# Kernel tuning notes

Hardware: AMD Instinct MI355X
Metric: run time of the kernel (lower is better)

The kernel has to match this reference:

```python
import jax, jax.numpy as jnp
import numpy as np

NUM_USERS = 100000
NUM_ITEMS = 50000
EMB_DIM = 128
NUM_LAYERS = 3
NUM_EDGES = 2000000
BATCH = 8192
REG = 1e-4


def setup_inputs() -> dict:
    key = jax.random.key(0)
    ks = jax.random.split(key, 8)
    N = NUM_USERS + NUM_ITEMS
    user_emb = jax.random.normal(ks[0], (NUM_USERS, EMB_DIM), dtype=jnp.float32) * 0.01
    item_emb = jax.random.normal(ks[1], (NUM_ITEMS, EMB_DIM), dtype=jnp.float32) * 0.01
    edge_row = jax.random.randint(ks[2], (NUM_EDGES,), 0, N, dtype=jnp.int32)
    edge_col = jax.random.randint(ks[3], (NUM_EDGES,), 0, N, dtype=jnp.int32)
    # symmetric-normalized adjacency values are small positives
    edge_val = jax.random.uniform(ks[4], (NUM_EDGES,), dtype=jnp.float32) * 0.1
    user = jax.random.randint(ks[5], (BATCH,), 0, NUM_USERS, dtype=jnp.int32)
    pos = jax.random.randint(ks[6], (BATCH,), 0, NUM_ITEMS, dtype=jnp.int32)
    neg = jax.random.randint(ks[7], (BATCH,), 0, NUM_ITEMS, dtype=jnp.int32)
    return {"user_emb": user_emb, "item_emb": item_emb,
            "edge_row": edge_row, "edge_col": edge_col, "edge_val": edge_val,
            "user": user, "pos": pos, "neg": neg}


def _lightgcn_embedding(user_emb, item_emb, edge_row, edge_col, edge_val):
    N = user_emb.shape[0] + item_emb.shape[0]
    emb = jnp.concatenate([user_emb, item_emb], axis=0)  # [N, D]
    acc = emb
    for _ in range(NUM_LAYERS):
        # SpMM: out[r] += val * emb[c] for each edge (r, c)
        msg = emb[edge_col] * edge_val[:, None]  # [E, D]
        emb = jax.ops.segment_sum(msg, edge_row, num_segments=N)
        acc = acc + emb
    light = acc / jnp.float32(NUM_LAYERS + 1)  # mean over layer outputs
    return light[:NUM_USERS], light[NUM_USERS:]


def reference(user_emb, item_emb, edge_row, edge_col, edge_val, user, pos, neg):
    u_all, i_all = _lightgcn_embedding(user_emb, item_emb, edge_row, edge_col, edge_val)
    u_lat = u_all[user]          # [B, D]
    pos_lat = i_all[pos]
    neg_lat = i_all[neg]
    pos_score = jnp.sum(u_lat * pos_lat, axis=1)
    neg_score = jnp.sum(u_lat * neg_lat, axis=1)
    # L1 regularization on ego (layer-0) embeddings, scalar broadcast onto batch loss
    reg_loss = REG * (jnp.sum(jnp.abs(user_emb[user]))
                      + jnp.sum(jnp.abs(item_emb[pos]))
                      + jnp.sum(jnp.abs(item_emb[neg])))
    batch_loss = jax.nn.softplus(neg_score - pos_score) + reg_loss
    return batch_loss
```

## Files before the change

kernel.cpp:

```cpp
#include <hip/hip_runtime.h>
#include <hip/hip_bf16.h>

#define EMB_D 128
#define BSH 9
#define MAXBUCK 512
#define CHUNKP 4096

typedef float f32x2 __attribute__((ext_vector_type(2)));

__device__ __forceinline__ float bf16_raw_to_f(unsigned short h) {
    return __uint_as_float(((unsigned int)h) << 16);
}
__device__ __forceinline__ float sane(float v) {
    return (v == v && fabsf(v) < 256.0f) ? v : 0.0f;
}
__device__ __forceinline__ float load_f(const void* p, int isf32, size_t idx) {
    return isf32 ? ((const float*)p)[idx]
                 : bf16_raw_to_f(((const unsigned short*)p)[idx]);
}

__device__ __forceinline__ f32x2 cvt2_fp8(unsigned int w) {
    f32x2 r;
    asm("v_cvt_pk_f32_fp8 %0, %1" : "=v"(r) : "v"(w));
    return r;
}
__device__ __forceinline__ unsigned int enc2_fp8(float a, float b) {
    unsigned int r;
    asm("v_cvt_pk_fp8_f32 %0, %1, %2" : "=v"(r) : "v"(a), "v"(b));
    return r & 0xFFFFu;
}
__device__ __forceinline__ unsigned int fp8x4_enc(float a, float b, float c, float d) {
    return enc2_fp8(a, b) | (enc2_fp8(c, d) << 16);
}
__device__ __forceinline__ float fp8_dec_byte(unsigned int b) {
    return cvt2_fp8(b & 0xFFu).x;
}

__global__ void k_detect(const unsigned short* __restrict__ ue,
                         const unsigned short* __restrict__ ie,
                         const unsigned short* __restrict__ ev,
                         int* __restrict__ flags) {
    int a = blockIdx.x;
    const unsigned short* p = (a == 0) ? ue : (a == 1) ? ie : ev;
    int lane = threadIdx.x;
    int cnt = 0;
    #pragma unroll
    for (int k = 0; k < 16; ++k) {
        float v = bf16_raw_to_f(p[k * 64 + lane]);
        if (!(fabsf(v) < 1.0f)) cnt++;
    }
    #pragma unroll
    for (int off = 32; off > 0; off >>= 1)
        cnt += __shfl_down(cnt, off, 64);
    if (lane == 0) flags[a] = (cnt > 64) ? 1 : 0;
}

__global__ __launch_bounds__(256) void k_build_emb8(
        const void* __restrict__ ue, const void* __restrict__ ie,
        const int* __restrict__ flags,
        unsigned char* __restrict__ T, float* __restrict__ S,
        int NU, int N) {
    int gid = blockIdx.x * blockDim.x + threadIdx.x;
    int row = gid >> 5;
    if (row >= N) return;
    int l = gid & 31;
    const void* src; long r; int f;
    if (row < NU) { src = ue; r = row;      f = flags[0]; }
    else          { src = ie; r = row - NU; f = flags[1]; }
    float v0, v1, v2, v3;
    if (f) {
        float4 t = ((const float4*)src)[r * 32 + l];
        v0 = sane(t.x); v1 = sane(t.y); v2 = sane(t.z); v3 = sane(t.w);
    } else {
        ushort4 t = ((const ushort4*)src)[r * 32 + l];
        v0 = sane(bf16_raw_to_f(t.x)); v1 = sane(bf16_raw_to_f(t.y));
        v2 = sane(bf16_raw_to_f(t.z)); v3 = sane(bf16_raw_to_f(t.w));
    }
    float m = fmaxf(fmaxf(fabsf(v0), fabsf(v1)), fmaxf(fabsf(v2), fabsf(v3)));
    #pragma unroll
    for (int off = 1; off < 32; off <<= 1)
        m = fmaxf(m, __shfl_xor(m, off, 64));
    float enc = (m > 0.0f) ? 448.0f / m : 0.0f;
    ((unsigned int*)T)[(size_t)row * 32 + l] =
        fp8x4_enc(v0 * enc, v1 * enc, v2 * enc, v3 * enc);
    if (l == 0) S[row] = (m > 0.0f) ? m * (1.0f / 448.0f) : 0.0f;
}

__global__ void k_init_acc(const void* __restrict__ ue, const void* __restrict__ ie,
                           const int* __restrict__ flags,
                           const int* __restrict__ user, const int* __restrict__ pos,
                           const int* __restrict__ neg, int NU, int NI,
                           float* __restrict__ uacc, float* __restrict__ pacc,
                           float* __restrict__ nacc, float* __restrict__ regp) {
    __shared__ float sred[2];
    int b = blockIdx.x;
    int d = threadIdx.x;
    int ui = min(max(user[b], 0), NU - 1);
    int pi = min(max(pos[b],  0), NI - 1);
    int ni = min(max(neg[b],  0), NI - 1);
    int f0 = flags[0], f1 = flags[1];
    float u = sane(load_f(ue, f0, (size_t)ui * EMB_D + d));
    float p = sane(load_f(ie, f1, (size_t)pi * EMB_D + d));
    float n = sane(load_f(ie, f1, (size_t)ni * EMB_D + d));
    size_t o = (size_t)b * EMB_D + d;
    uacc[o] = u;
    pacc[o] = p;
    nacc[o] = n;
    float s = fabsf(u) + fabsf(p) + fabsf(n);
    #pragma unroll
    for (int off = 32; off > 0; off >>= 1)
        s += __shfl_down(s, off, 64);
    if ((d & 63) == 0) sred[d >> 6] = s;
    __syncthreads();
    if (d == 0) regp[b] = sred[0] + sred[1];
}

__global__ void k_reduce_reg(const float* __restrict__ regp, float* __restrict__ reg, int B) {
    __shared__ float ss[256];
    int t = threadIdx.x;
    float s = 0.0f;
    for (int i = t; i < B; i += 256) s += regp[i];
    ss[t] = s;
    __syncthreads();
    for (int off = 128; off > 0; off >>= 1) {
        if (t < off) ss[t] += ss[t + off];
        __syncthreads();
    }
    if (t == 0) reg[0] = ss[0];
}


__global__ __launch_bounds__(256) void k_part_count(const int* __restrict__ erow,
        int* __restrict__ bcnt, int E, int N, int nbuck, int NB) {
    __shared__ int lh[MAXBUCK];
    int b = blockIdx.x, t = threadIdx.x;
    for (int i = t; i < MAXBUCK; i += 256) lh[i] = 0;
    __syncthreads();
    int beg = b * CHUNKP;
    int cnt = min(CHUNKP, E - beg);
    for (int p = t; p < cnt; p += 256) {
        int r = min(max(erow[beg + p], 0), N - 1);
        atomicAdd(&lh[r >> BSH], 1);
    }
    __syncthreads();
    for (int i = t; i < nbuck; i += 256) bcnt[(long)i * NB + b] = lh[i];
}

__global__ void k_gscan1(const int* __restrict__ a, int* __restrict__ bsums, int L) {
    __shared__ int ss[256];
    int t = threadIdx.x;
    int base = blockIdx.x * 1024 + t * 4;
    int s = 0;
    #pragma unroll
    for (int j = 0; j < 4; ++j) {
        int idx = base + j;
        if (idx < L) s += a[idx];
    }
    ss[t] = s;
    __syncthreads();
    for (int off = 128; off > 0; off >>= 1) {
        if (t < off) ss[t] += ss[t + off];
        __syncthreads();
    }
    if (t == 0) bsums[blockIdx.x] = ss[0];
}

__global__ void k_gscan2(const int* __restrict__ bsums, int* __restrict__ boffs,
                         int nb, int* __restrict__ rowptrN) {
    __shared__ int ss[256];
    int t = threadIdx.x;
    int s = (t < nb) ? bsums[t] : 0;
    ss[t] = s;
    __syncthreads();
    for (int off = 1; off < 256; off <<= 1) {
        int v = (t >= off) ? ss[t - off] : 0;
        __syncthreads();
        ss[t] += v;
        __syncthreads();
    }
    if (t < nb) boffs[t] = ss[t] - s;
    if (t == 255) *rowptrN = ss[255];
}

__global__ void k_gscan3(int* __restrict__ a, const int* __restrict__ boffs, int L) {
    __shared__ int ss[256];
    int t = threadIdx.x;
    int base = blockIdx.x * 1024 + t * 4;
    int c[4];
    int s = 0;
    #pragma unroll
    for (int j = 0; j < 4; ++j) {
        int idx = base + j;
        c[j] = (idx < L) ? a[idx] : 0;
        s += c[j];
    }
    ss[t] = s;
    __syncthreads();
    for (int off = 1; off < 256; off <<= 1) {
        int v = (t >= off) ? ss[t - off] : 0;
        __syncthreads();
        ss[t] += v;
        __syncthreads();
    }
    int run = boffs[blockIdx.x] + ss[t] - s;
    #pragma unroll
    for (int j = 0; j < 4; ++j) {
        int idx = base + j;
        if (idx < L) a[idx] = run;
        run += c[j];
    }
}

__global__ __launch_bounds__(256) void k_part_scatter(
        const int* __restrict__ erow, const int* __restrict__ ecol,
        const void* __restrict__ eval, const int* __restrict__ flags,
        const int* __restrict__ boff, uint2* __restrict__ part,
        int E, int N, int nbuck, int NB) {
    __shared__ uint2 lrec[CHUNKP];
    __shared__ unsigned short lidx[CHUNKP];
    __shared__ int hist[MAXBUCK];
    __shared__ int bstart[MAXBUCK];
    __shared__ int ss[256];
    int b = blockIdx.x, t = threadIdx.x;
    int beg = b * CHUNKP;
    int cnt = min(CHUNKP, E - beg);
    for (int i = t; i < MAXBUCK; i += 256) hist[i] = 0;
    __syncthreads();
    int f2 = flags[2];
    for (int p = t; p < cnt; p += 256) {
        int e = beg + p;
        int r = min(max(erow[e], 0), N - 1);
        int c = min(max(ecol[e], 0), N - 1);
        float v = sane(load_f(eval, f2, e));
        if (v < 0.0f) v = 0.0f;
        unsigned int u = __float_as_uint(v);
        unsigned int vb = ((u + 0x10000u) >> 17) & 0x3FFFu;
        lrec[p] = make_uint2((unsigned int)r, ((unsigned int)c << 14) | vb);
        atomicAdd(&hist[r >> BSH], 1);
    }
    __syncthreads();
    int c0 = hist[2 * t], c1 = hist[2 * t + 1];
    int s = c0 + c1;
    ss[t] = s;
    __syncthreads();
    for (int off = 1; off < 256; off <<= 1) {
        int v = (t >= off) ? ss[t - off] : 0;
        __syncthreads();
        ss[t] += v;
        __syncthreads();
    }
    int eb = ss[t] - s;
    bstart[2 * t] = eb;
    bstart[2 * t + 1] = eb + c0;
    hist[2 * t] = eb;
    hist[2 * t + 1] = eb + c0;
    __syncthreads();
    for (int p = t; p < cnt; p += 256) {
        int bin = (int)(lrec[p].x >> BSH);
        int pos = atomicAdd(&hist[bin], 1);
        lidx[pos] = (unsigned short)p;
    }
    __syncthreads();
    for (int i = t; i < nbuck; i += 256)
        hist[i] = boff[(long)i * NB + b] - bstart[i];
    __syncthreads();
    for (int p = t; p < cnt; p += 256) {
        uint2 rec = lrec[lidx[p]];
        int bin = (int)(rec.x >> BSH);
        part[hist[bin] + p] = rec;
    }
}

__global__ __launch_bounds__(256) void k_build_csr(
        const uint2* __restrict__ part, const int* __restrict__ boff,
        int* __restrict__ row_ptr, unsigned int* __restrict__ sedge,
        int E, int N, int NB, int nbuck) {
    __shared__ int rcnt[512];
    __shared__ int rstart[512];
    __shared__ int rcur[512];
    __shared__ int ss[256];
    int bin = blockIdx.x, t = threadIdx.x;
    int base = boff[(long)bin * NB];
    int next = (bin + 1 < nbuck) ? boff[(long)(bin + 1) * NB] : E;
    int cnt = next - base;
    int r0 = bin << BSH;
    int nrows = min(512, N - r0);
    rcnt[2 * t] = 0; rcnt[2 * t + 1] = 0;
    __syncthreads();
    for (int i = t; i < cnt; i += 256)
        atomicAdd(&rcnt[part[base + i].x - r0], 1);
    __syncthreads();
    int c0 = rcnt[2 * t], c1 = rcnt[2 * t + 1];
    int s = c0 + c1;
    ss[t] = s;
    __syncthreads();
    for (int off = 1; off < 256; off <<= 1) {
        int v = (t >= off) ? ss[t - off] : 0;
        __syncthreads();
        ss[t] += v;
        __syncthreads();
    }
    int eb = ss[t] - s;
    rstart[2 * t] = eb; rstart[2 * t + 1] = eb + c0;
    rcur[2 * t]   = eb; rcur[2 * t + 1]   = eb + c0;
    __syncthreads();
    for (int j = t; j < nrows; j += 256)
        row_ptr[r0 + j] = base + rstart[j];
    for (int i = t; i < cnt; i += 256) {
        uint2 rec = part[base + i];
        int pos = atomicAdd(&rcur[rec.x - r0], 1);
        sedge[base + pos] = rec.y;
    }
}


__global__ void k_zero_flags(int* __restrict__ f, int words) {
    int i = blockIdx.x * blockDim.x + threadIdx.x;
    if (i < words) f[i] = 0;
}

__global__ void k_mark_batch(const int* __restrict__ user, const int* __restrict__ pos,
                             const int* __restrict__ neg, int NU, int NI, int B,
                             unsigned char* __restrict__ flag3,
                             unsigned char* __restrict__ flag2) {
    int b = blockIdx.x * blockDim.x + threadIdx.x;
    if (b >= B) return;
    int ui = min(max(user[b], 0), NU - 1);
    int pi = NU + min(max(pos[b], 0), NI - 1);
    int ni = NU + min(max(neg[b], 0), NI - 1);
    flag3[ui] = 1; flag3[pi] = 1; flag3[ni] = 1;
    flag2[ui] = 1; flag2[pi] = 1; flag2[ni] = 1;
}

__global__ void k_mark_nbrs(const int* __restrict__ row_ptr,
                            const unsigned int* __restrict__ sedge,
                            const unsigned char* __restrict__ flag3,
                            unsigned char* __restrict__ flag2, int N) {
    int r = blockIdx.x * blockDim.x + threadIdx.x;
    if (r >= N || !flag3[r]) return;
    int beg = row_ptr[r], end = row_ptr[r + 1];
    for (int i = beg; i < end; ++i)
        flag2[sedge[i] >> 14] = 1;
}


__global__ void k_spmm_csr8(const unsigned char* __restrict__ T,
                            const float* __restrict__ S,
                            unsigned char* __restrict__ Td,
                            float* __restrict__ Sd,
                            const int* __restrict__ row_ptr,
                            const unsigned int* __restrict__ sedge, int N,
                            const unsigned char* __restrict__ skipf, int use_skip) {
    int row = blockIdx.x * (blockDim.x >> 6) + (threadIdx.x >> 6);
    if (row >= N) return;
    if (use_skip && skipf[row] == 0) return;
    int lane = threadIdx.x & 63;
    int sub = lane >> 3;
    int sl  = lane & 7;
    int beg = row_ptr[row], end = row_ptr[row + 1];
    float a[16];
    #pragma unroll
    for (int j = 0; j < 16; ++j) a[j] = 0.0f;
    int i = beg + sub;
    for (; i + 8 < end; i += 16) {
        unsigned int se0 = sedge[i];
        unsigned int se1 = sedge[i + 8];
        unsigned int c0 = se0 >> 14, c1 = se1 >> 14;
        uint4 h0 = ((const uint4*)(T + (size_t)c0 * EMB_D))[sl];
        uint4 h1 = ((const uint4*)(T + (size_t)c1 * EMB_D))[sl];
        float vs0 = __uint_as_float((se0 & 0x3FFFu) << 17) * S[c0];
        float vs1 = __uint_as_float((se1 & 0x3FFFu) << 17) * S[c1];
        f32x2 d;
        d = cvt2_fp8(h0.x);       a[0] += vs0 * d.x;  a[1] += vs0 * d.y;
        d = cvt2_fp8(h0.x >> 16); a[2] += vs0 * d.x;  a[3] += vs0 * d.y;
        d = cvt2_fp8(h0.y);       a[4] += vs0 * d.x;  a[5] += vs0 * d.y;
        d = cvt2_fp8(h0.y >> 16); a[6] += vs0 * d.x;  a[7] += vs0 * d.y;
        d = cvt2_fp8(h0.z);       a[8] += vs0 * d.x;  a[9] += vs0 * d.y;
        d = cvt2_fp8(h0.z >> 16); a[10] += vs0 * d.x; a[11] += vs0 * d.y;
        d = cvt2_fp8(h0.w);       a[12] += vs0 * d.x; a[13] += vs0 * d.y;
        d = cvt2_fp8(h0.w >> 16); a[14] += vs0 * d.x; a[15] += vs0 * d.y;
        d = cvt2_fp8(h1.x);       a[0] += vs1 * d.x;  a[1] += vs1 * d.y;
        d = cvt2_fp8(h1.x >> 16); a[2] += vs1 * d.x;  a[3] += vs1 * d.y;
        d = cvt2_fp8(h1.y);       a[4] += vs1 * d.x;  a[5] += vs1 * d.y;
        d = cvt2_fp8(h1.y >> 16); a[6] += vs1 * d.x;  a[7] += vs1 * d.y;
        d = cvt2_fp8(h1.z);       a[8] += vs1 * d.x;  a[9] += vs1 * d.y;
        d = cvt2_fp8(h1.z >> 16); a[10] += vs1 * d.x; a[11] += vs1 * d.y;
        d = cvt2_fp8(h1.w);       a[12] += vs1 * d.x; a[13] += vs1 * d.y;
        d = cvt2_fp8(h1.w >> 16); a[14] += vs1 * d.x; a[15] += vs1 * d.y;
    }
    if (i < end) {
        unsigned int se = sedge[i];
        unsigned int c = se >> 14;
        uint4 h = ((const uint4*)(T + (size_t)c * EMB_D))[sl];
        float vs = __uint_as_float((se & 0x3FFFu) << 17) * S[c];
        f32x2 d;
        d = cvt2_fp8(h.x);       a[0] += vs * d.x;  a[1] += vs * d.y;
        d = cvt2_fp8(h.x >> 16); a[2] += vs * d.x;  a[3] += vs * d.y;
        d = cvt2_fp8(h.y);       a[4] += vs * d.x;  a[5] += vs * d.y;
        d = cvt2_fp8(h.y >> 16); a[6] += vs * d.x;  a[7] += vs * d.y;
        d = cvt2_fp8(h.z);       a[8] += vs * d.x;  a[9] += vs * d.y;
        d = cvt2_fp8(h.z >> 16); a[10] += vs * d.x; a[11] += vs * d.y;
        d = cvt2_fp8(h.w);       a[12] += vs * d.x; a[13] += vs * d.y;
        d = cvt2_fp8(h.w >> 16); a[14] += vs * d.x; a[15] += vs * d.y;
    }
    #pragma unroll
    for (int j = 0; j < 16; ++j) {
        a[j] += __shfl_xor(a[j], 8, 64);
        a[j] += __shfl_xor(a[j], 16, 64);
        a[j] += __shfl_xor(a[j], 32, 64);
    }
    float m = 0.0f;
    #pragma unroll
    for (int j = 0; j < 16; ++j) m = fmaxf(m, fabsf(a[j]));
    m = fmaxf(m, __shfl_xor(m, 1, 64));
    m = fmaxf(m, __shfl_xor(m, 2, 64));
    m = fmaxf(m, __shfl_xor(m, 4, 64));
    if (sub == 0) {
        float enc = (m > 0.0f) ? 448.0f / m : 0.0f;
        uint4 w;
        w.x = fp8x4_enc(a[0] * enc,  a[1] * enc,  a[2] * enc,  a[3] * enc);
        w.y = fp8x4_enc(a[4] * enc,  a[5] * enc,  a[6] * enc,  a[7] * enc);
        w.z = fp8x4_enc(a[8] * enc,  a[9] * enc,  a[10] * enc, a[11] * enc);
        w.w = fp8x4_enc(a[12] * enc, a[13] * enc, a[14] * enc, a[15] * enc);
        ((uint4*)(Td + (size_t)row * EMB_D))[sl] = w;
        if (lane == 0) Sd[row] = (m > 0.0f) ? m * (1.0f / 448.0f) : 0.0f;
    }
}

__global__ void k_gather_add8(const unsigned char* __restrict__ T,
                              const float* __restrict__ S,
                              const int* __restrict__ user, const int* __restrict__ pos,
                              const int* __restrict__ neg,
                              float* __restrict__ uacc, float* __restrict__ pacc,
                              float* __restrict__ nacc, int NU, int NI) {
    int b = blockIdx.x;
    int d = threadIdx.x;
    int ui = min(max(user[b], 0), NU - 1);
    int pi = NU + min(max(pos[b], 0), NI - 1);
    int ni = NU + min(max(neg[b], 0), NI - 1);
    size_t o = (size_t)b * EMB_D + d;
    uacc[o] += fp8_dec_byte(T[(size_t)ui * EMB_D + d]) * S[ui];
    pacc[o] += fp8_dec_byte(T[(size_t)pi * EMB_D + d]) * S[pi];
    nacc[o] += fp8_dec_byte(T[(size_t)ni * EMB_D + d]) * S[ni];
}

__global__ void k_final(const float* __restrict__ uacc, const float* __restrict__ pacc,
                        const float* __restrict__ nacc, const float* __restrict__ reg,
                        float* __restrict__ out) {
    int b = blockIdx.x;
    int l = threadIdx.x;
    const float2* u2 = (const float2*)(uacc + (size_t)b * EMB_D);
    const float2* p2 = (const float2*)(pacc + (size_t)b * EMB_D);
    const float2* n2 = (const float2*)(nacc + (size_t)b * EMB_D);
    float2 u = u2[l], p = p2[l], n = n2[l];
    float ps = u.x * p.x + u.y * p.y;
    float ns = u.x * n.x + u.y * n.y;
    #pragma unroll
    for (int off = 32; off > 0; off >>= 1) {
        ps += __shfl_down(ps, off, 64);
        ns += __shfl_down(ns, off, 64);
    }
    if (l == 0) {
        float x = (ns - ps) * 0.0625f;
        float sp = fmaxf(x, 0.0f) + log1pf(expf(-fabsf(x)));
        out[b] = sp + 1e-4f * reg[0];
    }
}

extern "C" void kernel_launch(void* const* d_in, const int* in_sizes, int n_in,
                              void* d_out, int out_size, void* d_ws, size_t ws_size,
                              hipStream_t stream) {
    const void* ue   = d_in[0];
    const void* ie   = d_in[1];
    const int*  erow = (const int*)d_in[2];
    const int*  ecol = (const int*)d_in[3];
    const void* ev   = d_in[4];
    const int*  user = (const int*)d_in[5];
    const int*  pos  = (const int*)d_in[6];
    const int*  neg  = (const int*)d_in[7];

    int NU = in_sizes[0] / EMB_D;
    int NI = in_sizes[1] / EMB_D;
    int N  = NU + NI;
    int E  = in_sizes[2];
    int B  = in_sizes[5];

    int nbuck = (N + ((1 << BSH) - 1)) >> BSH;
    int NBp   = (E + CHUNKP - 1) / CHUNKP;
    int L     = nbuck * NBp;
    int nbL   = (L + 1023) / 1024;

    size_t BACC = (size_t)B * EMB_D * sizeof(float);
    size_t T8   = (size_t)N * EMB_D;
    size_t SC   = (((size_t)N * sizeof(float)) + 15) & ~15ull;
    size_t NI4  = ((size_t)(N + 1) * sizeof(int) + 15) & ~15ull;
    size_t L4   = ((size_t)L * sizeof(int) + 15) & ~15ull;
    size_t Npad = ((size_t)N + 15) & ~15ull;
    char* w = (char*)d_ws;
    int*   flags   = (int*)w;
    float* reg     = (float*)(w + 64);
    float* uacc    = (float*)(w + 256);
    float* pacc    = (float*)(w + 256 + BACC);
    float* nacc    = (float*)(w + 256 + 2 * BACC);
    char*  q       = w + 256 + 3 * BACC;
    float* regp    = (float*)q;             q += (size_t)B * sizeof(float);
    int*   row_ptr = (int*)q;               q += NI4;
    uint2* part    = (uint2*)q;             q += (size_t)E * sizeof(uint2);
    int*   bcnt    = (int*)q;               q += L4;
    int*   bsums   = (int*)q;               q += 1024;
    int*   boffs   = (int*)q;               q += 1024;
    unsigned char* flag3 = (unsigned char*)q; q += Npad;
    unsigned char* flag2 = (unsigned char*)q; q += Npad;
    unsigned int* sedge = (unsigned int*)q; q += (size_t)E * sizeof(unsigned int);
    unsigned char* Ta = (unsigned char*)q;  q += T8;
    float*         Sa = (float*)q;          q += SC;
    unsigned char* Tb = (unsigned char*)q;  q += T8;
    float*         Sb = (float*)q;

    const int thr = 256;
    float* out = (float*)d_out;

    k_detect<<<3, 64, 0, stream>>>((const unsigned short*)ue, (const unsigned short*)ie,
                                   (const unsigned short*)ev, flags);
    k_build_emb8<<<(N * 32 + thr - 1) / thr, thr, 0, stream>>>(ue, ie, flags, Ta, Sa, NU, N);
    k_init_acc<<<B, EMB_D, 0, stream>>>(ue, ie, flags, user, pos, neg, NU, NI,
                                        uacc, pacc, nacc, regp);
    k_reduce_reg<<<1, 256, 0, stream>>>(regp, reg, B);

    int fwords = (int)((2 * Npad) / 4);
    k_zero_flags<<<(fwords + thr - 1) / thr, thr, 0, stream>>>((int*)flag3, fwords);
    k_mark_batch<<<(B + thr - 1) / thr, thr, 0, stream>>>(user, pos, neg, NU, NI, B,
                                                          flag3, flag2);

    k_part_count<<<NBp, 256, 0, stream>>>(erow, bcnt, E, N, nbuck, NBp);
    k_gscan1<<<nbL, 256, 0, stream>>>(bcnt, bsums, L);
    k_gscan2<<<1, 256, 0, stream>>>(bsums, boffs, nbL, row_ptr + N);
    k_gscan3<<<nbL, 256, 0, stream>>>(bcnt, boffs, L);
    k_part_scatter<<<NBp, 256, 0, stream>>>(erow, ecol, ev, flags, bcnt, part, E, N, nbuck, NBp);
    k_build_csr<<<nbuck, 256, 0, stream>>>(part, bcnt, row_ptr, sedge, E, N, NBp, nbuck);

    k_mark_nbrs<<<(N + thr - 1) / thr, thr, 0, stream>>>(row_ptr, sedge, flag3, flag2, N);

    int rows_per_block = thr / 64;
    int sgrid = (N + rows_per_block - 1) / rows_per_block;

    k_spmm_csr8<<<sgrid, thr, 0, stream>>>(Ta, Sa, Tb, Sb, row_ptr, sedge, N, flag2, 0);
    k_gather_add8<<<B, EMB_D, 0, stream>>>(Tb, Sb, user, pos, neg, uacc, pacc, nacc, NU, NI);
    k_spmm_csr8<<<sgrid, thr, 0, stream>>>(Tb, Sb, Ta, Sa, row_ptr, sedge, N, flag2, 1);
    k_gather_add8<<<B, EMB_D, 0, stream>>>(Ta, Sa, user, pos, neg, uacc, pacc, nacc, NU, NI);
    k_spmm_csr8<<<sgrid, thr, 0, stream>>>(Ta, Sa, Tb, Sb, row_ptr, sedge, N, flag3, 1);
    k_gather_add8<<<B, EMB_D, 0, stream>>>(Tb, Sb, user, pos, neg, uacc, pacc, nacc, NU, NI);

    k_final<<<B, 64, 0, stream>>>(uacc, pacc, nacc, reg, out);
}
```

Before: 454.5 us.

## Keep per-layer fp8 outputs and fuse gathers with final loss; split partition records

The three per-layer batch gather-add kernels and the final scoring kernel are replaced by a single kernel that reads the ego embedding plus three separately stored layer outputs and computes the scores and softplus directly. This removes the float batch accumulators and several launches. The bucket-partition records are split into a 4-byte column/value array and a 2-byte local-row array, cutting partition traffic. The partition chunk is halved, which doubles the chunk count, so gscan2 now handles four entries per thread. The cost is two extra fp8 embedding buffers in workspace.

```diff
diff --git a/kernel.cpp b/kernel.cpp
--- a/kernel.cpp
+++ b/kernel.cpp
@@ -4,7 +4,7 @@
 #define EMB_D 128
 #define BSH 9
 #define MAXBUCK 512
-#define CHUNKP 4096
+#define CHUNKP 2048
 
 typedef float f32x2 __attribute__((ext_vector_type(2)));
 
@@ -86,12 +86,11 @@
     if (l == 0) S[row] = (m > 0.0f) ? m * (1.0f / 448.0f) : 0.0f;
 }
 
-__global__ void k_init_acc(const void* __restrict__ ue, const void* __restrict__ ie,
-                           const int* __restrict__ flags,
-                           const int* __restrict__ user, const int* __restrict__ pos,
-                           const int* __restrict__ neg, int NU, int NI,
-                           float* __restrict__ uacc, float* __restrict__ pacc,
-                           float* __restrict__ nacc, float* __restrict__ regp) {
+__global__ void k_reg(const void* __restrict__ ue, const void* __restrict__ ie,
+                      const int* __restrict__ flags,
+                      const int* __restrict__ user, const int* __restrict__ pos,
+                      const int* __restrict__ neg, int NU, int NI,
+                      float* __restrict__ regp) {
     __shared__ float sred[2];
     int b = blockIdx.x;
     int d = threadIdx.x;
@@ -102,10 +101,6 @@
     float u = sane(load_f(ue, f0, (size_t)ui * EMB_D + d));
     float p = sane(load_f(ie, f1, (size_t)pi * EMB_D + d));
     float n = sane(load_f(ie, f1, (size_t)ni * EMB_D + d));
-    size_t o = (size_t)b * EMB_D + d;
-    uacc[o] = u;
-    pacc[o] = p;
-    nacc[o] = n;
     float s = fabsf(u) + fabsf(p) + fabsf(n);
     #pragma unroll
     for (int off = 32; off > 0; off >>= 1)
@@ -169,7 +164,14 @@
                          int nb, int* __restrict__ rowptrN) {
     __shared__ int ss[256];
     int t = threadIdx.x;
-    int s = (t < nb) ? bsums[t] : 0;
+    int base = t * 4;
+    int c[4];
+    int s = 0;
+    #pragma unroll
+    for (int j = 0; j < 4; ++j) {
+        c[j] = (base + j < nb) ? bsums[base + j] : 0;
+        s += c[j];
+    }
     ss[t] = s;
     __syncthreads();
     for (int off = 1; off < 256; off <<= 1) {
@@ -178,7 +180,12 @@
         ss[t] += v;
         __syncthreads();
     }
-    if (t < nb) boffs[t] = ss[t] - s;
+    int run = ss[t] - s;
+    #pragma unroll
+    for (int j = 0; j < 4; ++j) {
+        if (base + j < nb) boffs[base + j] = run;
+        run += c[j];
+    }
     if (t == 255) *rowptrN = ss[255];
 }
 
@@ -214,7 +221,8 @@
 __global__ __launch_bounds__(256) void k_part_scatter(
         const int* __restrict__ erow, const int* __restrict__ ecol,
         const void* __restrict__ eval, const int* __restrict__ flags,
-        const int* __restrict__ boff, uint2* __restrict__ part,
+        const int* __restrict__ boff,
+        unsigned int* __restrict__ part_cv, unsigned short* __restrict__ part_r,
         int E, int N, int nbuck, int NB) {
     __shared__ uint2 lrec[CHUNKP];
     __shared__ unsigned short lidx[CHUNKP];
@@ -267,12 +275,16 @@
     for (int p = t; p < cnt; p += 256) {
         uint2 rec = lrec[lidx[p]];
         int bin = (int)(rec.x >> BSH);
-        part[hist[bin] + p] = rec;
+        int o = hist[bin] + p;
+        part_cv[o] = rec.y;
+        part_r[o] = (unsigned short)(rec.x & 511u);
     }
 }
 
 __global__ __launch_bounds__(256) void k_build_csr(
-        const uint2* __restrict__ part, const int* __restrict__ boff,
+        const unsigned int* __restrict__ part_cv,
+        const unsigned short* __restrict__ part_r,
+        const int* __restrict__ boff,
         int* __restrict__ row_ptr, unsigned int* __restrict__ sedge,
         int E, int N, int NB, int nbuck) {
     __shared__ int rcnt[512];
@@ -288,7 +300,7 @@
     rcnt[2 * t] = 0; rcnt[2 * t + 1] = 0;
     __syncthreads();
     for (int i = t; i < cnt; i += 256)
-        atomicAdd(&rcnt[part[base + i].x - r0], 1);
+        atomicAdd(&rcnt[part_r[base + i]], 1);
     __syncthreads();
     int c0 = rcnt[2 * t], c1 = rcnt[2 * t + 1];
     int s = c0 + c1;
@@ -307,9 +319,9 @@
     for (int j = t; j < nrows; j += 256)
         row_ptr[r0 + j] = base + rstart[j];
     for (int i = t; i < cnt; i += 256) {
-        uint2 rec = part[base + i];
-        int pos = atomicAdd(&rcur[rec.x - r0], 1);
-        sedge[base + pos] = rec.y;
+        int pr = part_r[base + i];
+        int pos = atomicAdd(&rcur[pr], 1);
+        sedge[base + pos] = part_cv[base + i];
     }
 }
 
@@ -427,41 +439,47 @@
     }
 }
 
-__global__ void k_gather_add8(const unsigned char* __restrict__ T,
-                              const float* __restrict__ S,
-                              const int* __restrict__ user, const int* __restrict__ pos,
-                              const int* __restrict__ neg,
-                              float* __restrict__ uacc, float* __restrict__ pacc,
-                              float* __restrict__ nacc, int NU, int NI) {
+__global__ void k_gather_final(
+        const void* __restrict__ ue, const void* __restrict__ ie,
+        const int* __restrict__ flags,
+        const int* __restrict__ user, const int* __restrict__ pos,
+        const int* __restrict__ neg, int NU, int NI,
+        const unsigned char* __restrict__ T1, const float* __restrict__ S1,
+        const unsigned char* __restrict__ T2, const float* __restrict__ S2,
+        const unsigned char* __restrict__ T3, const float* __restrict__ S3,
+        const float* __restrict__ reg, float* __restrict__ out) {
+    __shared__ float sps[2], sns[2];
     int b = blockIdx.x;
     int d = threadIdx.x;
     int ui = min(max(user[b], 0), NU - 1);
-    int pi = NU + min(max(pos[b], 0), NI - 1);
-    int ni = NU + min(max(neg[b], 0), NI - 1);
-    size_t o = (size_t)b * EMB_D + d;
-    uacc[o] += fp8_dec_byte(T[(size_t)ui * EMB_D + d]) * S[ui];
-    pacc[o] += fp8_dec_byte(T[(size_t)pi * EMB_D + d]) * S[pi];
-    nacc[o] += fp8_dec_byte(T[(size_t)ni * EMB_D + d]) * S[ni];
-}
-
-__global__ void k_final(const float* __restrict__ uacc, const float* __restrict__ pacc,
-                        const float* __restrict__ nacc, const float* __restrict__ reg,
-                        float* __restrict__ out) {
-    int b = blockIdx.x;
-    int l = threadIdx.x;
-    const float2* u2 = (const float2*)(uacc + (size_t)b * EMB_D);
-    const float2* p2 = (const float2*)(pacc + (size_t)b * EMB_D);
-    const float2* n2 = (const float2*)(nacc + (size_t)b * EMB_D);
-    float2 u = u2[l], p = p2[l], n = n2[l];
-    float ps = u.x * p.x + u.y * p.y;
-    float ns = u.x * n.x + u.y * n.y;
+    int pi = min(max(pos[b],  0), NI - 1);
+    int ni = min(max(neg[b],  0), NI - 1);
+    size_t ru = (size_t)ui;
+    size_t rp = (size_t)NU + pi;
+    size_t rn = (size_t)NU + ni;
+    int f0 = flags[0], f1 = flags[1];
+    float u = sane(load_f(ue, f0, ru * EMB_D + d))
+            + fp8_dec_byte(T1[ru * EMB_D + d]) * S1[ru]
+            + fp8_dec_byte(T2[ru * EMB_D + d]) * S2[ru]
+            + fp8_dec_byte(T3[ru * EMB_D + d]) * S3[ru];
+    float p = sane(load_f(ie, f1, (size_t)pi * EMB_D + d))
+            + fp8_dec_byte(T1[rp * EMB_D + d]) * S1[rp]
+            + fp8_dec_byte(T2[rp * EMB_D + d]) * S2[rp]
+            + fp8_dec_byte(T3[rp * EMB_D + d]) * S3[rp];
+    float n = sane(load_f(ie, f1, (size_t)ni * EMB_D + d))
+            + fp8_dec_byte(T1[rn * EMB_D + d]) * S1[rn]
+            + fp8_dec_byte(T2[rn * EMB_D + d]) * S2[rn]
+            + fp8_dec_byte(T3[rn * EMB_D + d]) * S3[rn];
+    float ps = u * p, ns = u * n;
     #pragma unroll
     for (int off = 32; off > 0; off >>= 1) {
         ps += __shfl_down(ps, off, 64);
         ns += __shfl_down(ns, off, 64);
     }
-    if (l == 0) {
-        float x = (ns - ps) * 0.0625f;
+    if ((d & 63) == 0) { sps[d >> 6] = ps; sns[d >> 6] = ns; }
+    __syncthreads();
+    if (d == 0) {
+        float x = ((sns[0] + sns[1]) - (sps[0] + sps[1])) * 0.0625f;
         float sp = fmaxf(x, 0.0f) + log1pf(expf(-fabsf(x)));
         out[b] = sp + 1e-4f * reg[0];
     }
@@ -490,32 +508,34 @@
     int L     = nbuck * NBp;
     int nbL   = (L + 1023) / 1024;
 
-    size_t BACC = (size_t)B * EMB_D * sizeof(float);
     size_t T8   = (size_t)N * EMB_D;
     size_t SC   = (((size_t)N * sizeof(float)) + 15) & ~15ull;
     size_t NI4  = ((size_t)(N + 1) * sizeof(int) + 15) & ~15ull;
     size_t L4   = ((size_t)L * sizeof(int) + 15) & ~15ull;
+    size_t E2   = (((size_t)E * 2) + 15) & ~15ull;
     size_t Npad = ((size_t)N + 15) & ~15ull;
     char* w = (char*)d_ws;
     int*   flags   = (int*)w;
     float* reg     = (float*)(w + 64);
-    float* uacc    = (float*)(w + 256);
-    float* pacc    = (float*)(w + 256 + BACC);
-    float* nacc    = (float*)(w + 256 + 2 * BACC);
-    char*  q       = w + 256 + 3 * BACC;
+    char*  q       = w + 256;
     float* regp    = (float*)q;             q += (size_t)B * sizeof(float);
     int*   row_ptr = (int*)q;               q += NI4;
-    uint2* part    = (uint2*)q;             q += (size_t)E * sizeof(uint2);
+    unsigned int*   part_cv = (unsigned int*)q;   q += (size_t)E * 4;
+    unsigned short* part_r  = (unsigned short*)q; q += E2;
     int*   bcnt    = (int*)q;               q += L4;
-    int*   bsums   = (int*)q;               q += 1024;
-    int*   boffs   = (int*)q;               q += 1024;
+    int*   bsums   = (int*)q;               q += 4096;
+    int*   boffs   = (int*)q;               q += 4096;
     unsigned char* flag3 = (unsigned char*)q; q += Npad;
     unsigned char* flag2 = (unsigned char*)q; q += Npad;
-    unsigned int* sedge = (unsigned int*)q; q += (size_t)E * sizeof(unsigned int);
+    unsigned int* sedge = (unsigned int*)q; q += (size_t)E * 4;
     unsigned char* Ta = (unsigned char*)q;  q += T8;
     float*         Sa = (float*)q;          q += SC;
-    unsigned char* Tb = (unsigned char*)q;  q += T8;
-    float*         Sb = (float*)q;
+    unsigned char* T1 = (unsigned char*)q;  q += T8;
+    float*         S1 = (float*)q;          q += SC;
+    unsigned char* T2 = (unsigned char*)q;  q += T8;
+    float*         S2 = (float*)q;          q += SC;
+    unsigned char* T3 = (unsigned char*)q;  q += T8;
+    float*         S3 = (float*)q;
 
     const int thr = 256;
     float* out = (float*)d_out;
@@ -523,8 +543,7 @@
     k_detect<<<3, 64, 0, stream>>>((const unsigned short*)ue, (const unsigned short*)ie,
                                    (const unsigned short*)ev, flags);
     k_build_emb8<<<(N * 32 + thr - 1) / thr, thr, 0, stream>>>(ue, ie, flags, Ta, Sa, NU, N);
-    k_init_acc<<<B, EMB_D, 0, stream>>>(ue, ie, flags, user, pos, neg, NU, NI,
-                                        uacc, pacc, nacc, regp);
+    k_reg<<<B, EMB_D, 0, stream>>>(ue, ie, flags, user, pos, neg, NU, NI, regp);
     k_reduce_reg<<<1, 256, 0, stream>>>(regp, reg, B);
 
     int fwords = (int)((2 * Npad) / 4);
@@ -536,20 +555,20 @@
     k_gscan1<<<nbL, 256, 0, stream>>>(bcnt, bsums, L);
     k_gscan2<<<1, 256, 0, stream>>>(bsums, boffs, nbL, row_ptr + N);
     k_gscan3<<<nbL, 256, 0, stream>>>(bcnt, boffs, L);
-    k_part_scatter<<<NBp, 256, 0, stream>>>(erow, ecol, ev, flags, bcnt, part, E, N, nbuck, NBp);
-    k_build_csr<<<nbuck, 256, 0, stream>>>(part, bcnt, row_ptr, sedge, E, N, NBp, nbuck);
+    k_part_scatter<<<NBp, 256, 0, stream>>>(erow, ecol, ev, flags, bcnt,
+                                            part_cv, part_r, E, N, nbuck, NBp);
+    k_build_csr<<<nbuck, 256, 0, stream>>>(part_cv, part_r, bcnt, row_ptr, sedge,
+                                           E, N, NBp, nbuck);
 
     k_mark_nbrs<<<(N + thr - 1) / thr, thr, 0, stream>>>(row_ptr, sedge, flag3, flag2, N);
 
     int rows_per_block = thr / 64;
     int sgrid = (N + rows_per_block - 1) / rows_per_block;
 
-    k_spmm_csr8<<<sgrid, thr, 0, stream>>>(Ta, Sa, Tb, Sb, row_ptr, sedge, N, flag2, 0);
-    k_gather_add8<<<B, EMB_D, 0, stream>>>(Tb, Sb, user, pos, neg, uacc, pacc, nacc, NU, NI);
-    k_spmm_csr8<<<sgrid, thr, 0, stream>>>(Tb, Sb, Ta, Sa, row_ptr, sedge, N, flag2, 1);
-    k_gather_add8<<<B, EMB_D, 0, stream>>>(Ta, Sa, user, pos, neg, uacc, pacc, nacc, NU, NI);
-    k_spmm_csr8<<<sgrid, thr, 0, stream>>>(Ta, Sa, Tb, Sb, row_ptr, sedge, N, flag3, 1);
-    k_gather_add8<<<B, EMB_D, 0, stream>>>(Tb, Sb, user, pos, neg, uacc, pacc, nacc, NU, NI);
-
-    k_final<<<B, 64, 0, stream>>>(uacc, pacc, nacc, reg, out);
-}
+    k_spmm_csr8<<<sgrid, thr, 0, stream>>>(Ta, Sa, T1, S1, row_ptr, sedge, N, flag2, 0);
+    k_spmm_csr8<<<sgrid, thr, 0, stream>>>(T1, S1, T2, S2, row_ptr, sedge, N, flag2, 1);
+    k_spmm_csr8<<<sgrid, thr, 0, stream>>>(T2, S2, T3, S3, row_ptr, sedge, N, flag3, 1);
+
+    k_gather_final<<<B, EMB_D, 0, stream>>>(ue, ie, flags, user, pos, neg, NU, NI,
+                                            T1, S1, T2, S2, T3, S3, reg, out);
+}
```

Measured after the change: 441.5 us. 1.03x faster.
